# Performance work log

Hardware: AMD Instinct MI355X
Metric: run time of the kernel (lower is better)

The kernel has to match this reference:

```python
import jax, jax.numpy as jnp
import numpy as np

B, N = 32, 8192
NUM_CLASSES = 40
SA1_DIMS = (3, 64, 64, 128)      # grouped relative xyz only (in_channels=3 -> no extra features)
SA2_DIMS = (131, 128, 128, 256)  # 128 SA1 features + 3 relative xyz
LOC_DIMS = (256, 256, 512, 1024)
GLOB_DIMS = (1024, 512, 256)


def _fps(xyz, m):
    """Farthest point sampling. xyz: [B,N,3] -> indices [B,m] (first index is point 0)."""
    b, n, _ = xyz.shape
    big = jnp.asarray(1e10, xyz.dtype)

    def step(carry, _):
        dists, last = carry                                   # [B,N], [B]
        p = jnp.take_along_axis(xyz, last[:, None, None], axis=1)  # [B,1,3]
        d = jnp.sum((xyz - p) ** 2, axis=-1)                  # [B,N]
        dists = jnp.minimum(dists, d)
        nxt = jnp.argmax(dists, axis=-1).astype(jnp.int32)
        return (dists, nxt), nxt

    init = (jnp.full((b, n), big, xyz.dtype), jnp.zeros((b,), jnp.int32))
    _, rest = jax.lax.scan(step, init, None, length=m - 1)    # [m-1,B]
    return jnp.concatenate([jnp.zeros((b, 1), jnp.int32), rest.T], axis=1)


def _ball_query(xyz, new_xyz, radius, k):
    """First-k points within radius of each centroid, padded with the first hit (CUDA ball_query semantics)."""
    d2 = jnp.sum((new_xyz[:, :, None, :] - xyz[:, None, :, :]) ** 2, axis=-1)  # [B,M,N]
    valid = d2 < radius * radius
    n = xyz.shape[1]
    ar = jnp.arange(n, dtype=jnp.int32)
    order_key = jnp.where(valid, ar, ar + n)                  # valid points sort first, in index order
    _, idx = jax.lax.top_k(-order_key, k)                     # [B,M,K] first-k valid indices
    num_valid = jnp.sum(valid, axis=-1)                       # [B,M]
    idx = jnp.where(jnp.arange(k) < num_valid[..., None], idx, idx[..., :1])
    return idx.astype(jnp.int32)


_gather = jax.vmap(lambda p, i: p[i])  # p:[N,C], i:[M,K] -> [M,K,C], vmapped over batch


def _sa(xyz, feats, m, radius, k, ws, bs):
    """PointNetSAModule: FPS -> ball query -> group (relative xyz [+feat]) -> SharedMLP -> max over K."""
    cidx = _fps(xyz, m)
    new_xyz = jnp.take_along_axis(xyz, cidx[:, :, None], axis=1)   # [B,m,3]
    idx = _ball_query(xyz, new_xyz, radius, k)                     # [B,m,k]
    x = _gather(xyz, idx) - new_xyz[:, :, None, :]                 # [B,m,k,3]
    if feats is not None:
        x = jnp.concatenate([x, _gather(feats, idx)], axis=-1)
    for w, b in zip(ws, bs):  # Conv2d(1x1)+BN(eval, folded)+ReLU
        x = jax.nn.relu(jnp.einsum('bmkc,oc->bmko', x, w) + b)
    return new_xyz, jnp.max(x, axis=2)                             # [B,m,C_out]


def _forward(points, sa1_w0, sa1_b0, sa1_w1, sa1_b1, sa1_w2, sa1_b2,
             sa2_w0, sa2_b0, sa2_w1, sa2_b1, sa2_w2, sa2_b2,
             loc_w0, loc_b0, loc_w1, loc_b1, loc_w2, loc_b2,
             glob_w0, glob_b0, glob_w1, glob_b1, cls_w, cls_b):
    xyz = jnp.transpose(points, (0, 2, 1))                         # [B,N,3]
    new_xyz, feats = _sa(xyz, None, 512, 0.2, 32,
                         (sa1_w0, sa1_w1, sa1_w2), (sa1_b0, sa1_b1, sa1_b2))
    _, feats = _sa(new_xyz, feats, 128, 0.4, 64,
                   (sa2_w0, sa2_w1, sa2_w2), (sa2_b0, sa2_b1, sa2_b2))
    x = feats                                                      # [B,128,256]
    for w, b in ((loc_w0, loc_b0), (loc_w1, loc_b1), (loc_w2, loc_b2)):
        x = jax.nn.relu(jnp.einsum('bnc,oc->bno', x, w) + b)       # SharedMLP (Conv1d+BN+ReLU)
    x = jnp.max(x, axis=1)                                         # global max-pool -> [B,1024]
    for w, b in ((glob_w0, glob_b0), (glob_w1, glob_b1)):          # MLP (dropout in eval = identity)
        x = jax.nn.relu(x @ w.T + b)
    return x @ cls_w.T + cls_b                                     # cls_logits [B,40]


def setup_inputs() -> dict:
    key = jax.random.key(0)
    ks = iter(jax.random.split(key, 64))
    inp = {}
    # unit-cube point cloud so radii 0.2/0.4 are geometrically meaningful
    inp['points'] = jax.random.uniform(next(ks), (B, 3, N), jnp.float32, -1.0, 1.0)

    def lin(co, ci):
        return jax.random.normal(next(ks), (co, ci), jnp.float32) / np.sqrt(ci)

    for name, dims in (('sa1', SA1_DIMS), ('sa2', SA2_DIMS), ('loc', LOC_DIMS)):
        for i in range(len(dims) - 1):
            inp[f'{name}_w{i}'] = lin(dims[i + 1], dims[i])
            inp[f'{name}_b{i}'] = 0.01 * jax.random.normal(next(ks), (dims[i + 1],), jnp.float32)
    for i in range(2):
        inp[f'glob_w{i}'] = lin(GLOB_DIMS[i + 1], GLOB_DIMS[i])
        inp[f'glob_b{i}'] = 0.01 * jax.random.normal(next(ks), (GLOB_DIMS[i + 1],), jnp.float32)
    inp['cls_w'] = lin(NUM_CLASSES, GLOB_DIMS[-1])
    inp['cls_b'] = jnp.zeros((NUM_CLASSES,), jnp.float32)
    return inp


def reference(points, sa1_w0, sa1_b0, sa1_w1, sa1_b1, sa1_w2, sa1_b2,
              sa2_w0, sa2_b0, sa2_w1, sa2_b1, sa2_w2, sa2_b2,
              loc_w0, loc_b0, loc_w1, loc_b1, loc_w2, loc_b2,
              glob_w0, glob_b0, glob_w1, glob_b1, cls_w, cls_b):
    return _forward(points, sa1_w0, sa1_b0, sa1_w1, sa1_b1, sa1_w2, sa1_b2,
                    sa2_w0, sa2_b0, sa2_w1, sa2_b1, sa2_w2, sa2_b2,
                    loc_w0, loc_b0, loc_w1, loc_b1, loc_w2, loc_b2,
                    glob_w0, glob_b0, glob_w1, glob_b1, cls_w, cls_b)
```

## Files before the change

### kernel.cpp

```cpp
#include <hip/hip_runtime.h>
#include <hip/hip_bf16.h>
#include <cstdint>

#define CDIV(a,b) (((a)+(b)-1)/(b))

typedef short s8v __attribute__((ext_vector_type(8)));
typedef float f4v __attribute__((ext_vector_type(4)));
typedef float f2v __attribute__((ext_vector_type(2)));

__device__ __forceinline__ unsigned short f2bf_bits(float v) {
  __hip_bfloat16 b = __float2bfloat16(v);
  unsigned short u; __builtin_memcpy(&u, &b, 2);
  return u;
}
__device__ __forceinline__ void bsplit(float v, unsigned short& h, unsigned short& l) {
  __hip_bfloat16 hb = __float2bfloat16(v);
  float hf = __bfloat162float(hb);
  unsigned short hu; __builtin_memcpy(&hu, &hb, 2);
  h = hu;
  l = f2bf_bits(v - hf);
}

__device__ __forceinline__ void gl2lds16(const void* g, void* l, int lane) {
#if __has_builtin(__builtin_amdgcn_global_load_lds)
  __builtin_amdgcn_global_load_lds(
      (const __attribute__((address_space(1))) unsigned int*)g,
      (__attribute__((address_space(3))) unsigned int*)l, 16, 0, 0);
#else
  ((uint4*)l)[lane] = *(const uint4*)g;
#endif
}

__device__ __forceinline__ void agpr_put(float& slot, float v) {
  asm volatile("v_accvgpr_write_b32 %0, %1" : "=a"(slot) : "v"(v));
}
__device__ __forceinline__ float agpr_get(const float& slot) {
  float v;
  asm volatile("v_accvgpr_read_b32 %0, %1" : "=v"(v) : "a"(slot));
  return v;
}

__device__ __forceinline__ f2v pk_add(f2v a, f2v b) {
  f2v d; asm("v_pk_add_f32 %0, %1, %2" : "=v"(d) : "v"(a), "v"(b)); return d;
}
__device__ __forceinline__ f2v pk_mul(f2v a, f2v b) {
  f2v d; asm("v_pk_mul_f32 %0, %1, %2" : "=v"(d) : "v"(a), "v"(b)); return d;
}
__device__ __forceinline__ f2v pk_fma(f2v a, f2v b, f2v c) {
  f2v d; asm("v_pk_fma_f32 %0, %1, %2, %3" : "=v"(d) : "v"(a), "v"(b), "v"(c)); return d;
}

template<int C>
__device__ __forceinline__ unsigned dpp32(unsigned v) {
  return (unsigned)__builtin_amdgcn_update_dpp((int)v, (int)v, C, 0xF, 0xF, false);
}
template<int C>
__device__ __forceinline__ unsigned long long red_key(unsigned long long pk) {
  unsigned lo = dpp32<C>((unsigned)pk);
  unsigned hi = dpp32<C>((unsigned)(pk >> 32));
  unsigned long long p2 = ((unsigned long long)hi << 32) | lo;
  return (p2 > pk) ? p2 : pk;
}

template<int NPTS, int MOUT, int NTHR>
__global__ __launch_bounds__(NTHR, 1) void fps_kernel(
    const float* __restrict__ pts, int bstride, int cstride,
    int* __restrict__ out_idx)
{
  constexpr int PPT = NPTS / NTHR;
  constexpr int NP2 = PPT / 2;
  constexpr int NW  = NTHR / 64;
  const int b = blockIdx.x, t = threadIdx.x;
  const int lane = t & 63, wid = t >> 6;
  const float* px = pts + (size_t)b * bstride;
  const float* py = px + cstride;
  const float* pz = px + 2 * cstride;
  __shared__ float s_x[NPTS], s_y[NPTS], s_z[NPTS];
  __shared__ unsigned long long s_key[2][NW];
  __shared__ int s_out[MOUT];

  float ax[PPT], ay[PPT], az[PPT];
  f2v dsv[NP2];
#pragma unroll
  for (int j = 0; j < PPT; ++j) {
    int i = t + j * NTHR;
    float x = px[i], y = py[i], z = pz[i];
    s_x[i] = x; s_y[i] = y; s_z[i] = z;
    agpr_put(ax[j], x); agpr_put(ay[j], y); agpr_put(az[j], z);
  }
#pragma unroll
  for (int q = 0; q < NP2; ++q) dsv[q] = (f2v){1e10f, 1e10f};
  if (t == 0) s_out[0] = 0;
  float lx = px[0], ly = py[0], lz = pz[0];
  __syncthreads();

  for (int it = 1; it < MOUT; ++it) {
    const int pb = it & 1;
    const f2v nlx = (f2v){-lx, -lx};
    const f2v nly = (f2v){-ly, -ly};
    const f2v nlz = (f2v){-lz, -lz};
    float bestv = -1.0f; int bestj = 0;
#pragma unroll
    for (int q = 0; q < NP2; ++q) {
      f2v x2, y2, z2;
      x2.x = agpr_get(ax[2 * q]); x2.y = agpr_get(ax[2 * q + 1]);
      y2.x = agpr_get(ay[2 * q]); y2.y = agpr_get(ay[2 * q + 1]);
      z2.x = agpr_get(az[2 * q]); z2.y = agpr_get(az[2 * q + 1]);
      f2v dx = pk_add(x2, nlx);
      f2v dy = pk_add(y2, nly);
      f2v dz = pk_add(z2, nlz);
      f2v d2 = pk_fma(dz, dz, pk_fma(dy, dy, pk_mul(dx, dx)));
      float nd0 = fminf(dsv[q].x, d2.x);
      float nd1 = fminf(dsv[q].y, d2.y);
      dsv[q].x = nd0; dsv[q].y = nd1;
      if (nd0 > bestv) { bestv = nd0; bestj = 2 * q; }
      if (nd1 > bestv) { bestv = nd1; bestj = 2 * q + 1; }
    }
    const int besti = t + bestj * NTHR;
    unsigned long long pk =
        ((unsigned long long)__float_as_uint(bestv) << 32) | (unsigned)(~(unsigned)besti);
    pk = red_key<0x111>(pk);
    pk = red_key<0x112>(pk);
    pk = red_key<0x114>(pk);
    pk = red_key<0x118>(pk);
    pk = red_key<0x142>(pk);
    pk = red_key<0x143>(pk);
    if (lane == 63) s_key[pb][wid] = pk;
    __syncthreads();
    unsigned long long ck = s_key[pb][lane & (NW - 1)];
    if (NW >= 2) ck = red_key<0x111>(ck);
    if (NW >= 4) ck = red_key<0x112>(ck);
    if (NW >= 8) ck = red_key<0x114>(ck);
    const int widx = (int)(~(unsigned)__builtin_amdgcn_readlane((int)(unsigned)ck, NW - 1));
    lx = s_x[widx]; ly = s_y[widx]; lz = s_z[widx];
    if (t == 0) s_out[it] = widx;
  }
  __syncthreads();
  for (int i = t; i < MOUT; i += NTHR)
    out_idx[(size_t)b * MOUT + i] = s_out[i];
}

__global__ void gatherc_kernel(
    const float* __restrict__ pts, int bstride, int cstride,
    const int* __restrict__ cidx, int M,
    float* __restrict__ aos, float* __restrict__ soa)
{
  const int b = blockIdx.x, t = threadIdx.x;
  const int i = cidx[(size_t)b * M + t];
  const float* p = pts + (size_t)b * bstride;
  float x = p[i], y = p[cstride + i], z = p[2 * cstride + i];
  size_t g = (size_t)b * M + t;
  aos[g * 3 + 0] = x; aos[g * 3 + 1] = y; aos[g * 3 + 2] = z;
  soa[(size_t)b * 3 * M + t]         = x;
  soa[(size_t)b * 3 * M + M + t]     = y;
  soa[(size_t)b * 3 * M + 2 * M + t] = z;
}

template<int NPTS, int KNB, int MC>
__global__ __launch_bounds__(64) void ballq_wave(
    const float* __restrict__ pts, int bstride, int cstride,
    const float* __restrict__ cents, int* __restrict__ out, float r2)
{
  constexpr int NCH = NPTS / 64;
  const int g = blockIdx.x;
  const int b = g / MC;
  const int lane = threadIdx.x;
  const float* px = pts + (size_t)b * bstride;
  const float* py = px + cstride;
  const float* pz = px + 2 * cstride;
  const float cx = cents[g * 3 + 0], cy = cents[g * 3 + 1], cz = cents[g * 3 + 2];
  __shared__ int s_idx[KNB];
  float nx = px[lane], ny = py[lane], nz = pz[lane];
  int base = 0;
  for (int c = 0; c < NCH; ++c) {
    float X = nx, Y = ny, Z = nz;
    if (c + 1 < NCH) {
      int i2 = (c + 1) * 64 + lane;
      nx = px[i2]; ny = py[i2]; nz = pz[i2];
    }
    float dx = X - cx, dy = Y - cy, dz = Z - cz;
    bool valid = (dx * dx + dy * dy + dz * dz) < r2;
    unsigned long long mask = __ballot(valid);
    int rank = __popcll(mask & ((1ull << lane) - 1ull));
    int pos = base + rank;
    if (valid && pos < KNB) s_idx[pos] = c * 64 + lane;
    base += __popcll(mask);
    if (base >= KNB) break;
  }
  int total = base < KNB ? base : KNB;
  int first = s_idx[0];
  if (lane < KNB)
    out[(size_t)g * KNB + lane] = (lane < total) ? s_idx[lane] : first;
}

__global__ __launch_bounds__(256) void sa1l1_kernel(
    const float* __restrict__ pts, const int* __restrict__ idx1,
    const float* __restrict__ cents,
    const float* __restrict__ w0, const float* __restrict__ b0,
    unsigned short* __restrict__ Yh, unsigned short* __restrict__ Yl,
    int g0, int nrows)
{
  __shared__ float sw[192];
  __shared__ float sb[64];
  const int tid = threadIdx.x;
  if (tid < 192) sw[tid] = w0[tid];
  else sb[tid - 192] = b0[tid - 192];
  __syncthreads();
  const int r = blockIdx.x * 64 + (tid >> 2);
  if (r >= nrows) return;
  const int q = tid & 3;
  const int gl = r >> 5, j = r & 31, gg = g0 + gl, b = gg >> 9;
  const int i = idx1[(size_t)gg * 32 + j];
  const float* px = pts + (size_t)b * 24576;
  const float x = px[i]         - cents[gg * 3 + 0];
  const float y = px[8192 + i]  - cents[gg * 3 + 1];
  const float z = px[16384 + i] - cents[gg * 3 + 2];
  union { unsigned short us[16]; uint4 v[2]; } ph, pl;
#pragma unroll
  for (int u = 0; u < 16; ++u) {
    const int o = q * 16 + u;
    float v = sw[o * 3] * x + sw[o * 3 + 1] * y + sw[o * 3 + 2] * z + sb[o];
    v = fmaxf(v, 0.f);
    bsplit(v, ph.us[u], pl.us[u]);
  }
  uint4* dh = (uint4*)(Yh + (size_t)r * 64 + q * 16);
  uint4* dl = (uint4*)(Yl + (size_t)r * 64 + q * 16);
  dh[0] = ph.v[0]; dh[1] = ph.v[1];
  dl[0] = pl.v[0]; dl[1] = pl.v[1];
}

__global__ void gather2p_kernel(
    const float* __restrict__ nx1_aos,
    const unsigned short* __restrict__ f1h, const unsigned short* __restrict__ f1l,
    const int* __restrict__ idx2, const float* __restrict__ nx2_aos,
    unsigned short* __restrict__ Xh, unsigned short* __restrict__ Xl, int g0)
{
  const int r = blockIdx.x * 4 + threadIdx.y;
  const int lane = threadIdx.x;
  int gl = r >> 6, j = r & 63;
  int gg = g0 + gl;
  int b  = gg >> 7;
  int i  = idx2[(size_t)gg * 64 + j];
  int p  = b * 512 + i;
  size_t ro = (size_t)r * 160;
  const int slot = lane & 31;
  const bool isL = lane >= 32;
  unsigned short* dst = isL ? Xl : Xh;
  const unsigned short* f1 = isL ? f1l : f1h;
  if (slot < 16) {
    ((uint4*)(dst + ro))[slot] = ((const uint4*)(f1 + (size_t)p * 128))[slot];
  } else if (slot == 16) {
    union { unsigned short us[8]; uint4 v; } pk;
#pragma unroll
    for (int u = 0; u < 8; ++u) pk.us[u] = 0;
#pragma unroll
    for (int c = 0; c < 3; ++c) {
      float v = nx1_aos[(size_t)p * 3 + c] - nx2_aos[(size_t)gg * 3 + c];
      unsigned short h, l; bsplit(v, h, l);
      pk.us[c] = isL ? l : h;
    }
    ((uint4*)(dst + ro))[16] = pk.v;
  } else if (slot <= 19) {
    ((uint4*)(dst + ro))[slot] = make_uint4(0, 0, 0, 0);
  }
}

struct WSplitArgs {
  const float* src[9];
  unsigned short* h[9];
  unsigned short* l[9];
  int K[9];
  int KP[9];
  int perm[9];
  int cum[10];
};
__global__ void wsplit_all(WSplitArgs a) {
  int i = blockIdx.x * 256 + threadIdx.x;
  if (i >= a.cum[9]) return;
  int s = 0;
#pragma unroll
  for (int t = 1; t < 9; ++t) s += (i >= a.cum[t]);
  int local = i - a.cum[s];
  int KP = a.KP[s], K = a.K[s];
  int r = local / KP, k = local - r * KP;
  int oc;
  if (a.perm[s]) oc = (k < 128) ? k + 3 : (k < 131 ? k - 128 : -1);
  else           oc = (k < K) ? k : -1;
  float v = (oc >= 0) ? a.src[s][(size_t)r * K + oc] : 0.f;
  unsigned short hb, lb; bsplit(v, hb, lb);
  a.h[s][local] = hb; a.l[s][local] = lb;
}

template<int BN, int POOL>
__global__ __launch_bounds__(256, 1) void mfma_gemm(
    const unsigned short* __restrict__ Ah, const unsigned short* __restrict__ Al,
    const unsigned short* __restrict__ Wh, const unsigned short* __restrict__ Wl,
    const float* __restrict__ bias,
    unsigned short* __restrict__ Ch, unsigned short* __restrict__ Cl,
    float* __restrict__ Cf,
    unsigned short* __restrict__ Chp, unsigned short* __restrict__ Clp,
    int Kdim, int Ndim)
{
  constexpr int WTN = BN / 2, NT = WTN / 16;
  __shared__ unsigned short sA[2][128 * 32];
  __shared__ unsigned short sW[2][BN * 32];
  __shared__ float sPool[4][WTN];
  const int tid = threadIdx.x, lane = tid & 63, wid = tid >> 6;
  const int wm = wid & 1, wn = wid >> 1;
  const size_t bm0 = (size_t)blockIdx.y * 128;
  const int bn0 = blockIdx.x * BN;
  const int mn15 = lane & 15, kgrp = lane >> 4;

  f4v acc[4][NT];
#pragma unroll
  for (int a = 0; a < 4; ++a)
#pragma unroll
    for (int b = 0; b < NT; ++b) acc[a][b] = (f4v){0.f, 0.f, 0.f, 0.f};

  const int sc = lane & 3, srl = lane >> 2;

  for (int k0 = 0; k0 < Kdim; k0 += 32) {
#pragma unroll
    for (int hh = 0; hh < 2; ++hh) {
      const int R = wid * 32 + hh * 16;
      const int m = R + srl;
      const int kg = (sc - m - (m >> 2)) & 3;
      const size_t go = (bm0 + m) * (size_t)Kdim + k0 + kg * 8;
      gl2lds16(Ah + go, &sA[0][R * 32], lane);
      gl2lds16(Al + go, &sA[1][R * 32], lane);
    }
    if (BN == 128) {
#pragma unroll
      for (int hh = 0; hh < 2; ++hh) {
        const int R = wid * 32 + hh * 16;
        const int n = R + srl;
        const int kg = (sc - n - (n >> 2)) & 3;
        const size_t go = (size_t)(bn0 + n) * Kdim + k0 + kg * 8;
        gl2lds16(Wh + go, &sW[0][R * 32], lane);
        gl2lds16(Wl + go, &sW[1][R * 32], lane);
      }
    } else {
      const int R = wid * 16;
      const int n = R + srl;
      const int kg = (sc - n - (n >> 2)) & 3;
      const size_t go = (size_t)(bn0 + n) * Kdim + k0 + kg * 8;
      gl2lds16(Wh + go, &sW[0][R * 32], lane);
      gl2lds16(Wl + go, &sW[1][R * 32], lane);
    }
    __syncthreads();

    s8v af[2][4], bfr[2][NT];
#pragma unroll
    for (int mt = 0; mt < 4; ++mt) {
      const int m = wm * 64 + mt * 16 + mn15;
      const int cc = (kgrp + m + (m >> 2)) & 3;
      af[0][mt] = *(const s8v*)&sA[0][m * 32 + cc * 8];
      af[1][mt] = *(const s8v*)&sA[1][m * 32 + cc * 8];
    }
#pragma unroll
    for (int nt = 0; nt < NT; ++nt) {
      const int n = wn * WTN + nt * 16 + mn15;
      const int cc = (kgrp + n + (n >> 2)) & 3;
      bfr[0][nt] = *(const s8v*)&sW[0][n * 32 + cc * 8];
      bfr[1][nt] = *(const s8v*)&sW[1][n * 32 + cc * 8];
    }
#pragma unroll
    for (int mt = 0; mt < 4; ++mt)
#pragma unroll
      for (int nt = 0; nt < NT; ++nt) {
        acc[mt][nt] = __builtin_amdgcn_mfma_f32_16x16x32_bf16(af[0][mt], bfr[0][nt], acc[mt][nt], 0, 0, 0);
        acc[mt][nt] = __builtin_amdgcn_mfma_f32_16x16x32_bf16(af[0][mt], bfr[1][nt], acc[mt][nt], 0, 0, 0);
        acc[mt][nt] = __builtin_amdgcn_mfma_f32_16x16x32_bf16(af[1][mt], bfr[0][nt], acc[mt][nt], 0, 0, 0);
      }
    __syncthreads();
  }

  float bv[NT];
#pragma unroll
  for (int nt = 0; nt < NT; ++nt) bv[nt] = bias[bn0 + wn * WTN + nt * 16 + mn15];

  if (POOL == 0) {
#pragma unroll
    for (int mt = 0; mt < 4; ++mt)
#pragma unroll
      for (int nt = 0; nt < NT; ++nt) {
        const int n = bn0 + wn * WTN + nt * 16 + mn15;
#pragma unroll
        for (int r = 0; r < 4; ++r) {
          const size_t m = bm0 + wm * 64 + mt * 16 + (lane >> 4) * 4 + r;
          float v = fmaxf(acc[mt][nt][r] + bv[nt], 0.f);
          unsigned short h, l; bsplit(v, h, l);
          Ch[m * Ndim + n] = h;
          Cl[m * Ndim + n] = l;
        }
      }
  } else if (POOL == 32) {
#pragma unroll
    for (int gq = 0; gq < 2; ++gq)
#pragma unroll
      for (int nt = 0; nt < NT; ++nt) {
        float v = -1e30f;
#pragma unroll
        for (int mt = 2 * gq; mt < 2 * gq + 2; ++mt)
#pragma unroll
          for (int r = 0; r < 4; ++r) v = fmaxf(v, acc[mt][nt][r]);
        v = fmaxf(v + bv[nt], 0.f);
        v = fmaxf(v, __shfl_xor(v, 16, 64));
        v = fmaxf(v, __shfl_xor(v, 32, 64));
        if (lane < 16) {
          const int n = bn0 + wn * WTN + nt * 16 + mn15;
          const size_t row = bm0 / 32 + wm * 2 + gq;
          if (Chp) { unsigned short h, l; bsplit(v, h, l);
                     Chp[row * Ndim + n] = h; Clp[row * Ndim + n] = l; }
          if (Cf) Cf[row * Ndim + n] = v;
        }
      }
  } else if (POOL == 64) {
#pragma unroll
    for (int nt = 0; nt < NT; ++nt) {
      float v = -1e30f;
#pragma unroll
      for (int mt = 0; mt < 4; ++mt)
#pragma unroll
        for (int r = 0; r < 4; ++r) v = fmaxf(v, acc[mt][nt][r]);
      v = fmaxf(v + bv[nt], 0.f);
      v = fmaxf(v, __shfl_xor(v, 16, 64));
      v = fmaxf(v, __shfl_xor(v, 32, 64));
      if (lane < 16) {
        const int n = bn0 + wn * WTN + nt * 16 + mn15;
        const size_t row = bm0 / 64 + wm;
        if (Chp) { unsigned short h, l; bsplit(v, h, l);
                   Chp[row * Ndim + n] = h; Clp[row * Ndim + n] = l; }
        if (Cf) Cf[row * Ndim + n] = v;
      }
    }
  } else {
    float part[NT];
#pragma unroll
    for (int nt = 0; nt < NT; ++nt) {
      float v = -1e30f;
#pragma unroll
      for (int mt = 0; mt < 4; ++mt)
#pragma unroll
        for (int r = 0; r < 4; ++r) v = fmaxf(v, acc[mt][nt][r]);
      v = fmaxf(v + bv[nt], 0.f);
      v = fmaxf(v, __shfl_xor(v, 16, 64));
      v = fmaxf(v, __shfl_xor(v, 32, 64));
      part[nt] = v;
      if (lane < 16) sPool[wid][nt * 16 + mn15] = v;
    }
    __syncthreads();
    if (wm == 0 && lane < 16) {
#pragma unroll
      for (int nt = 0; nt < NT; ++nt) {
        float v = fmaxf(part[nt], sPool[wid + 1][nt * 16 + mn15]);
        const int n = bn0 + wn * WTN + nt * 16 + mn15;
        if (Cf) Cf[(size_t)(bm0 / 128) * Ndim + n] = v;
      }
    }
  }
}

__global__ __launch_bounds__(256) void head_kernel(
    const float* __restrict__ pooled,
    const float* __restrict__ w0, const float* __restrict__ b0,
    const float* __restrict__ w1, const float* __restrict__ b1,
    const float* __restrict__ wc, const float* __restrict__ bc,
    float* __restrict__ out)
{
  __shared__ float sx[1024];
  __shared__ float sy[512];
  __shared__ float sz[256];
  const int b = blockIdx.x, t = threadIdx.x;
  for (int i = t; i < 1024; i += 256) sx[i] = pooled[(size_t)b * 1024 + i];
  __syncthreads();
  for (int o = t; o < 512; o += 256) {
    const float4* w4 = (const float4*)(w0 + (size_t)o * 1024);
    const float4* x4 = (const float4*)sx;
    float acc = 0.f;
#pragma unroll 4
    for (int k = 0; k < 256; ++k) {
      float4 w = w4[k], x = x4[k];
      acc += w.x * x.x + w.y * x.y + w.z * x.z + w.w * x.w;
    }
    sy[o] = fmaxf(acc + b0[o], 0.f);
  }
  __syncthreads();
  if (t < 256) {
    const float4* w4 = (const float4*)(w1 + (size_t)t * 512);
    const float4* y4 = (const float4*)sy;
    float acc = 0.f;
#pragma unroll 4
    for (int k = 0; k < 128; ++k) {
      float4 w = w4[k], y = y4[k];
      acc += w.x * y.x + w.y * y.y + w.z * y.z + w.w * y.w;
    }
    sz[t] = fmaxf(acc + b1[t], 0.f);
  }
  __syncthreads();
  if (t < 40) {
    const float4* w4 = (const float4*)(wc + (size_t)t * 256);
    const float4* z4 = (const float4*)sz;
    float acc = 0.f;
#pragma unroll 4
    for (int k = 0; k < 64; ++k) {
      float4 w = w4[k], z = z4[k];
      acc += w.x * z.x + w.y * z.y + w.z * z.z + w.w * z.w;
    }
    out[(size_t)b * 40 + t] = acc + bc[t];
  }
}

extern "C" void kernel_launch(void* const* d_in, const int* in_sizes, int n_in,
                              void* d_out, int out_size, void* d_ws, size_t ws_size,
                              hipStream_t stream)
{
  (void)in_sizes; (void)n_in; (void)out_size; (void)ws_size;

  const float* points  = (const float*)d_in[0];
  const float* sa1_w[3] = {(const float*)d_in[1], (const float*)d_in[3], (const float*)d_in[5]};
  const float* sa1_b[3] = {(const float*)d_in[2], (const float*)d_in[4], (const float*)d_in[6]};
  const float* sa2_w[3] = {(const float*)d_in[7], (const float*)d_in[9], (const float*)d_in[11]};
  const float* sa2_b[3] = {(const float*)d_in[8], (const float*)d_in[10], (const float*)d_in[12]};
  const float* loc_w[3] = {(const float*)d_in[13], (const float*)d_in[15], (const float*)d_in[17]};
  const float* loc_b[3] = {(const float*)d_in[14], (const float*)d_in[16], (const float*)d_in[18]};
  const float* glob_w0 = (const float*)d_in[19];
  const float* glob_b0 = (const float*)d_in[20];
  const float* glob_w1 = (const float*)d_in[21];
  const float* glob_b1 = (const float*)d_in[22];
  const float* cls_w   = (const float*)d_in[23];
  const float* cls_b   = (const float*)d_in[24];

  char* base = (char*)d_ws;
  size_t off = 0;
  auto alloc = [&](size_t nbytes) -> void* {
    void* p = base + off;
    off += (nbytes + 255) & ~(size_t)255;
    return p;
  };

  const size_t XE = (size_t)65536 * 160;
  const size_t YE = (size_t)131072 * 64;
  unsigned short* Xh = (unsigned short*)alloc(XE * 2);
  unsigned short* Xl = (unsigned short*)alloc(XE * 2);
  unsigned short* Yh = (unsigned short*)alloc(YE * 2);
  unsigned short* Yl = (unsigned short*)alloc(YE * 2);
  unsigned short* f1h = (unsigned short*)alloc((size_t)16384 * 128 * 2);
  unsigned short* f1l = (unsigned short*)alloc((size_t)16384 * 128 * 2);
  unsigned short* f2h = (unsigned short*)alloc((size_t)4096 * 256 * 2);
  unsigned short* f2l = (unsigned short*)alloc((size_t)4096 * 256 * 2);

  const int  wrows[9] = {64, 64, 128, 128, 128, 256, 256, 512, 1024};
  const int  wK[9]    = {3, 64, 64, 131, 128, 128, 256, 256, 512};
  const int  wKP[9]   = {32, 64, 64, 160, 128, 128, 256, 256, 512};
  const float* wsrc[9] = {sa1_w[0], sa1_w[1], sa1_w[2],
                          sa2_w[0], sa2_w[1], sa2_w[2],
                          loc_w[0], loc_w[1], loc_w[2]};
  unsigned short *wph[9], *wpl[9];
  WSplitArgs wa;
  int cum = 0;
  for (int s = 0; s < 9; ++s) {
    size_t e = (size_t)wrows[s] * wKP[s];
    wph[s] = (unsigned short*)alloc(e * 2);
    wpl[s] = (unsigned short*)alloc(e * 2);
    wa.src[s] = wsrc[s]; wa.h[s] = wph[s]; wa.l[s] = wpl[s];
    wa.K[s] = wK[s]; wa.KP[s] = wKP[s]; wa.cum[s] = cum;
    wa.perm[s] = (s == 3) ? 1 : 0;
    cum += wrows[s] * wKP[s];
  }
  wa.cum[9] = cum;

  float* nx1_aos = (float*)alloc((size_t)32 * 512 * 3 * 4);
  float* nx1_soa = (float*)alloc((size_t)32 * 512 * 3 * 4);
  int*   cidx1   = (int*)  alloc((size_t)32 * 512 * 4);
  int*   idx1    = (int*)  alloc((size_t)32 * 512 * 32 * 4);
  float* nx2_aos = (float*)alloc((size_t)32 * 128 * 3 * 4);
  float* nx2_soa = (float*)alloc((size_t)32 * 128 * 3 * 4);
  int*   cidx2   = (int*)  alloc((size_t)32 * 128 * 4);
  int*   idx2    = (int*)  alloc((size_t)32 * 128 * 64 * 4);
  float* pooled  = (float*)alloc((size_t)32 * 1024 * 4);

  const float r2a = (float)(0.2 * 0.2);
  const float r2b = (float)(0.4 * 0.4);

  wsplit_all<<<CDIV(cum, 256), 256, 0, stream>>>(wa);

  fps_kernel<8192, 512, 512><<<32, 512, 0, stream>>>(points, 24576, 8192, cidx1);
  gatherc_kernel<<<32, 512, 0, stream>>>(points, 24576, 8192, cidx1, 512, nx1_aos, nx1_soa);
  ballq_wave<8192, 32, 512><<<32 * 512, 64, 0, stream>>>(points, 24576, 8192, nx1_aos, idx1, r2a);

  for (int c = 0; c < 4; ++c) {
    const int g0 = c * 4096;
    const int rows = 4096 * 32;
    sa1l1_kernel<<<CDIV(rows, 64), 256, 0, stream>>>(
        points, idx1, nx1_aos, sa1_w[0], sa1_b[0], Yh, Yl, g0, rows);
    mfma_gemm<64, 0><<<dim3(1, rows / 128), 256, 0, stream>>>(
        Yh, Yl, wph[1], wpl[1], sa1_b[1], Xh, Xl, nullptr, nullptr, nullptr, 64, 64);
    mfma_gemm<128, 32><<<dim3(1, rows / 128), 256, 0, stream>>>(
        Xh, Xl, wph[2], wpl[2], sa1_b[2], nullptr, nullptr, nullptr,
        f1h + (size_t)g0 * 128, f1l + (size_t)g0 * 128, 64, 128);
  }

  fps_kernel<512, 128, 256><<<32, 256, 0, stream>>>(nx1_soa, 1536, 512, cidx2);
  gatherc_kernel<<<32, 128, 0, stream>>>(nx1_soa, 1536, 512, cidx2, 128, nx2_aos, nx2_soa);
  ballq_wave<512, 64, 128><<<32 * 128, 64, 0, stream>>>(nx1_soa, 1536, 512, nx2_aos, idx2, r2b);

  for (int c = 0; c < 4; ++c) {
    const int g0 = c * 1024;
    const int rows = 1024 * 64;
    gather2p_kernel<<<dim3(rows / 4), dim3(64, 4), 0, stream>>>(
        nx1_aos, f1h, f1l, idx2, nx2_aos, Xh, Xl, g0);
    mfma_gemm<128, 0><<<dim3(1, rows / 128), 256, 0, stream>>>(
        Xh, Xl, wph[3], wpl[3], sa2_b[0], Yh, Yl, nullptr, nullptr, nullptr, 160, 128);
    mfma_gemm<128, 0><<<dim3(1, rows / 128), 256, 0, stream>>>(
        Yh, Yl, wph[4], wpl[4], sa2_b[1], Xh, Xl, nullptr, nullptr, nullptr, 128, 128);
    mfma_gemm<128, 64><<<dim3(2, rows / 128), 256, 0, stream>>>(
        Xh, Xl, wph[5], wpl[5], sa2_b[2], nullptr, nullptr, nullptr,
        f2h + (size_t)g0 * 256, f2l + (size_t)g0 * 256, 128, 256);
  }

  mfma_gemm<128, 0><<<dim3(2, 32), 256, 0, stream>>>(
      f2h, f2l, wph[6], wpl[6], loc_b[0], Yh, Yl, nullptr, nullptr, nullptr, 256, 256);
  mfma_gemm<128, 0><<<dim3(4, 32), 256, 0, stream>>>(
      Yh, Yl, wph[7], wpl[7], loc_b[1], Xh, Xl, nullptr, nullptr, nullptr, 256, 512);
  mfma_gemm<128, 128><<<dim3(8, 32), 256, 0, stream>>>(
      Xh, Xl, wph[8], wpl[8], loc_b[2], nullptr, nullptr, pooled, nullptr, nullptr, 512, 1024);

  head_kernel<<<32, 256, 0, stream>>>(pooled, glob_w0, glob_b0,
                                      glob_w1, glob_b1, cls_w, cls_b, (float*)d_out);
}
```

Measured before the change: 1.327 ms.

## Fuse SA1 MLP layers and max-pool into one kernel; single-wave FPS for SA2

Replaces the per-chunk SA1 pipeline (first-layer kernel plus two GEMM launches with global intermediates) with one kernel per 128-row tile. That kernel computes layer 0, runs both MFMA GEMMs through LDS, and max-pools over the 32 neighbours in registers. This removes global round-trips of the intermediate activations and 11 launches. It also runs the second FPS with one 64-thread wave, so the block-wide barrier and LDS reduction drop out, at the cost of less parallelism per batch.

```diff
diff --git a/kernel.cpp b/kernel.cpp
--- a/kernel.cpp
+++ b/kernel.cpp
@@ -71,7 +71,8 @@
   constexpr int NP2 = PPT / 2;
   constexpr int NW  = NTHR / 64;
   const int b = blockIdx.x, t = threadIdx.x;
-  const int lane = t & 63, wid = t >> 6;
+  const int lane = t & 63;
+  const int wid = t >> 6;
   const float* px = pts + (size_t)b * bstride;
   const float* py = px + cstride;
   const float* pz = px + 2 * cstride;
@@ -95,7 +96,6 @@
   __syncthreads();
 
   for (int it = 1; it < MOUT; ++it) {
-    const int pb = it & 1;
     const f2v nlx = (f2v){-lx, -lx};
     const f2v nly = (f2v){-ly, -ly};
     const f2v nlz = (f2v){-lz, -lz};
@@ -125,13 +125,19 @@
     pk = red_key<0x118>(pk);
     pk = red_key<0x142>(pk);
     pk = red_key<0x143>(pk);
-    if (lane == 63) s_key[pb][wid] = pk;
-    __syncthreads();
-    unsigned long long ck = s_key[pb][lane & (NW - 1)];
-    if (NW >= 2) ck = red_key<0x111>(ck);
-    if (NW >= 4) ck = red_key<0x112>(ck);
-    if (NW >= 8) ck = red_key<0x114>(ck);
-    const int widx = (int)(~(unsigned)__builtin_amdgcn_readlane((int)(unsigned)ck, NW - 1));
+    int widx;
+    if constexpr (NW == 1) {
+      widx = (int)(~(unsigned)__builtin_amdgcn_readlane((int)(unsigned)pk, 63));
+    } else {
+      const int pb = it & 1;
+      if (lane == 63) s_key[pb][wid] = pk;
+      __syncthreads();
+      unsigned long long ck = s_key[pb][lane & (NW - 1)];
+      if (NW >= 2) ck = red_key<0x111>(ck);
+      if (NW >= 4) ck = red_key<0x112>(ck);
+      if (NW >= 8) ck = red_key<0x114>(ck);
+      widx = (int)(~(unsigned)__builtin_amdgcn_readlane((int)(unsigned)ck, NW - 1));
+    }
     lx = s_x[widx]; ly = s_y[widx]; lz = s_z[widx];
     if (t == 0) s_out[it] = widx;
   }
@@ -193,40 +199,172 @@
     out[(size_t)g * KNB + lane] = (lane < total) ? s_idx[lane] : first;
 }
 
-__global__ __launch_bounds__(256) void sa1l1_kernel(
+__global__ __launch_bounds__(256, 1) void sa1_fused(
     const float* __restrict__ pts, const int* __restrict__ idx1,
     const float* __restrict__ cents,
     const float* __restrict__ w0, const float* __restrict__ b0,
-    unsigned short* __restrict__ Yh, unsigned short* __restrict__ Yl,
-    int g0, int nrows)
+    const unsigned short* __restrict__ w1h, const unsigned short* __restrict__ w1l,
+    const float* __restrict__ b1,
+    const unsigned short* __restrict__ w2h, const unsigned short* __restrict__ w2l,
+    const float* __restrict__ b2,
+    unsigned short* __restrict__ f1h, unsigned short* __restrict__ f1l)
 {
-  __shared__ float sw[192];
-  __shared__ float sb[64];
-  const int tid = threadIdx.x;
-  if (tid < 192) sw[tid] = w0[tid];
-  else sb[tid - 192] = b0[tid - 192];
-  __syncthreads();
-  const int r = blockIdx.x * 64 + (tid >> 2);
-  if (r >= nrows) return;
-  const int q = tid & 3;
-  const int gl = r >> 5, j = r & 31, gg = g0 + gl, b = gg >> 9;
-  const int i = idx1[(size_t)gg * 32 + j];
-  const float* px = pts + (size_t)b * 24576;
-  const float x = px[i]         - cents[gg * 3 + 0];
-  const float y = px[8192 + i]  - cents[gg * 3 + 1];
-  const float z = px[16384 + i] - cents[gg * 3 + 2];
-  union { unsigned short us[16]; uint4 v[2]; } ph, pl;
-#pragma unroll
-  for (int u = 0; u < 16; ++u) {
-    const int o = q * 16 + u;
-    float v = sw[o * 3] * x + sw[o * 3 + 1] * y + sw[o * 3 + 2] * z + sb[o];
-    v = fmaxf(v, 0.f);
-    bsplit(v, ph.us[u], pl.us[u]);
-  }
-  uint4* dh = (uint4*)(Yh + (size_t)r * 64 + q * 16);
-  uint4* dl = (uint4*)(Yl + (size_t)r * 64 + q * 16);
-  dh[0] = ph.v[0]; dh[1] = ph.v[1];
-  dl[0] = pl.v[0]; dl[1] = pl.v[1];
+  __shared__ __align__(16) unsigned short sY[2][128 * 72];
+  __shared__ __align__(16) unsigned short sZ[2][128 * 72];
+  __shared__ __align__(16) unsigned short sW[2][64 * 72];
+  __shared__ float sw0[192];
+  __shared__ float sb0[64];
+
+  const int tid = threadIdx.x, lane = tid & 63, wid = tid >> 6;
+  const int wm = wid & 1, wn = wid >> 1;
+  const int mn15 = lane & 15, kgrp = lane >> 4;
+  const int bk = blockIdx.x;
+
+  if (tid < 192) sw0[tid] = w0[tid];
+  else sb0[tid - 192] = b0[tid - 192];
+  for (int gi = tid; gi < 1024; gi += 256) {
+    const int pl = gi >> 9, idx = gi & 511;
+    const int n = idx >> 3, k8 = idx & 7;
+    const uint4 v = ((const uint4*)(pl ? w1l : w1h))[idx];
+    *(uint4*)&sW[pl][n * 72 + k8 * 8] = v;
+  }
+  __syncthreads();
+
+  {
+    const int rl = tid >> 1, half = tid & 1;
+    const int r = bk * 128 + rl;
+    const int gl = r >> 5, j = r & 31, b = gl >> 9;
+    const int i = idx1[(size_t)gl * 32 + j];
+    const float* px = pts + (size_t)b * 24576;
+    const float x = px[i]         - cents[gl * 3 + 0];
+    const float y = px[8192 + i]  - cents[gl * 3 + 1];
+    const float z = px[16384 + i] - cents[gl * 3 + 2];
+    union { unsigned short us[32]; uint4 v[4]; } ph, pl4;
+#pragma unroll
+    for (int u = 0; u < 32; ++u) {
+      const int o = half * 32 + u;
+      float v = sw0[o * 3] * x + sw0[o * 3 + 1] * y + sw0[o * 3 + 2] * z + sb0[o];
+      v = fmaxf(v, 0.f);
+      bsplit(v, ph.us[u], pl4.us[u]);
+    }
+    const int base = rl * 72 + half * 32;
+#pragma unroll
+    for (int g = 0; g < 4; ++g) {
+      *(uint4*)&sY[0][base + g * 8] = ph.v[g];
+      *(uint4*)&sY[1][base + g * 8] = pl4.v[g];
+    }
+  }
+  __syncthreads();
+
+  {
+    f4v acc[4][2];
+#pragma unroll
+    for (int a = 0; a < 4; ++a)
+#pragma unroll
+      for (int c = 0; c < 2; ++c) acc[a][c] = (f4v){0.f, 0.f, 0.f, 0.f};
+#pragma unroll
+    for (int kc = 0; kc < 2; ++kc) {
+      const int k0 = kc * 32;
+      s8v af[2][4], bf[2][2];
+#pragma unroll
+      for (int mt = 0; mt < 4; ++mt) {
+        const int m = wm * 64 + mt * 16 + mn15;
+        af[0][mt] = *(const s8v*)&sY[0][m * 72 + k0 + kgrp * 8];
+        af[1][mt] = *(const s8v*)&sY[1][m * 72 + k0 + kgrp * 8];
+      }
+#pragma unroll
+      for (int nt = 0; nt < 2; ++nt) {
+        const int n = wn * 32 + nt * 16 + mn15;
+        bf[0][nt] = *(const s8v*)&sW[0][n * 72 + k0 + kgrp * 8];
+        bf[1][nt] = *(const s8v*)&sW[1][n * 72 + k0 + kgrp * 8];
+      }
+#pragma unroll
+      for (int mt = 0; mt < 4; ++mt)
+#pragma unroll
+        for (int nt = 0; nt < 2; ++nt) {
+          acc[mt][nt] = __builtin_amdgcn_mfma_f32_16x16x32_bf16(af[0][mt], bf[0][nt], acc[mt][nt], 0, 0, 0);
+          acc[mt][nt] = __builtin_amdgcn_mfma_f32_16x16x32_bf16(af[0][mt], bf[1][nt], acc[mt][nt], 0, 0, 0);
+          acc[mt][nt] = __builtin_amdgcn_mfma_f32_16x16x32_bf16(af[1][mt], bf[0][nt], acc[mt][nt], 0, 0, 0);
+        }
+    }
+#pragma unroll
+    for (int nt = 0; nt < 2; ++nt) {
+      const int n = wn * 32 + nt * 16 + mn15;
+      const float bv = b1[n];
+#pragma unroll
+      for (int mt = 0; mt < 4; ++mt)
+#pragma unroll
+        for (int r = 0; r < 4; ++r) {
+          const int m = wm * 64 + mt * 16 + (lane >> 4) * 4 + r;
+          float v = fmaxf(acc[mt][nt][r] + bv, 0.f);
+          unsigned short h, l; bsplit(v, h, l);
+          sZ[0][m * 72 + n] = h;
+          sZ[1][m * 72 + n] = l;
+        }
+    }
+  }
+  __syncthreads();
+
+  for (int gi = tid; gi < 2048; gi += 256) {
+    const int pl = gi >> 10, idx = gi & 1023;
+    const int n = idx >> 3, k8 = idx & 7;
+    const uint4 v = ((const uint4*)(pl ? w2l : w2h))[idx];
+    *(uint4*)&sY[pl][n * 72 + k8 * 8] = v;
+  }
+  __syncthreads();
+
+  {
+    f4v acc[4][4];
+#pragma unroll
+    for (int a = 0; a < 4; ++a)
+#pragma unroll
+      for (int c = 0; c < 4; ++c) acc[a][c] = (f4v){0.f, 0.f, 0.f, 0.f};
+#pragma unroll
+    for (int kc = 0; kc < 2; ++kc) {
+      const int k0 = kc * 32;
+      s8v af[2][4], bf[2][4];
+#pragma unroll
+      for (int mt = 0; mt < 4; ++mt) {
+        const int m = wm * 64 + mt * 16 + mn15;
+        af[0][mt] = *(const s8v*)&sZ[0][m * 72 + k0 + kgrp * 8];
+        af[1][mt] = *(const s8v*)&sZ[1][m * 72 + k0 + kgrp * 8];
+      }
+#pragma unroll
+      for (int nt = 0; nt < 4; ++nt) {
+        const int n = wn * 64 + nt * 16 + mn15;
+        bf[0][nt] = *(const s8v*)&sY[0][n * 72 + k0 + kgrp * 8];
+        bf[1][nt] = *(const s8v*)&sY[1][n * 72 + k0 + kgrp * 8];
+      }
+#pragma unroll
+      for (int mt = 0; mt < 4; ++mt)
+#pragma unroll
+        for (int nt = 0; nt < 4; ++nt) {
+          acc[mt][nt] = __builtin_amdgcn_mfma_f32_16x16x32_bf16(af[0][mt], bf[0][nt], acc[mt][nt], 0, 0, 0);
+          acc[mt][nt] = __builtin_amdgcn_mfma_f32_16x16x32_bf16(af[0][mt], bf[1][nt], acc[mt][nt], 0, 0, 0);
+          acc[mt][nt] = __builtin_amdgcn_mfma_f32_16x16x32_bf16(af[1][mt], bf[0][nt], acc[mt][nt], 0, 0, 0);
+        }
+    }
+#pragma unroll
+    for (int gq = 0; gq < 2; ++gq)
+#pragma unroll
+      for (int nt = 0; nt < 4; ++nt) {
+        const int n = wn * 64 + nt * 16 + mn15;
+        float v = -1e30f;
+#pragma unroll
+        for (int mt = 2 * gq; mt < 2 * gq + 2; ++mt)
+#pragma unroll
+          for (int r = 0; r < 4; ++r) v = fmaxf(v, acc[mt][nt][r]);
+        v = fmaxf(v + b2[n], 0.f);
+        v = fmaxf(v, __shfl_xor(v, 16, 64));
+        v = fmaxf(v, __shfl_xor(v, 32, 64));
+        if (lane < 16) {
+          const size_t row = (size_t)bk * 4 + wm * 2 + gq;
+          unsigned short h, l; bsplit(v, h, l);
+          f1h[row * 128 + n] = h;
+          f1l[row * 128 + n] = l;
+        }
+      }
+  }
 }
 
 __global__ void gather2p_kernel(
@@ -589,19 +727,11 @@
   gatherc_kernel<<<32, 512, 0, stream>>>(points, 24576, 8192, cidx1, 512, nx1_aos, nx1_soa);
   ballq_wave<8192, 32, 512><<<32 * 512, 64, 0, stream>>>(points, 24576, 8192, nx1_aos, idx1, r2a);
 
-  for (int c = 0; c < 4; ++c) {
-    const int g0 = c * 4096;
-    const int rows = 4096 * 32;
-    sa1l1_kernel<<<CDIV(rows, 64), 256, 0, stream>>>(
-        points, idx1, nx1_aos, sa1_w[0], sa1_b[0], Yh, Yl, g0, rows);
-    mfma_gemm<64, 0><<<dim3(1, rows / 128), 256, 0, stream>>>(
-        Yh, Yl, wph[1], wpl[1], sa1_b[1], Xh, Xl, nullptr, nullptr, nullptr, 64, 64);
-    mfma_gemm<128, 32><<<dim3(1, rows / 128), 256, 0, stream>>>(
-        Xh, Xl, wph[2], wpl[2], sa1_b[2], nullptr, nullptr, nullptr,
-        f1h + (size_t)g0 * 128, f1l + (size_t)g0 * 128, 64, 128);
-  }
-
-  fps_kernel<512, 128, 256><<<32, 256, 0, stream>>>(nx1_soa, 1536, 512, cidx2);
+  sa1_fused<<<4096, 256, 0, stream>>>(
+      points, idx1, nx1_aos, sa1_w[0], sa1_b[0],
+      wph[1], wpl[1], sa1_b[1], wph[2], wpl[2], sa1_b[2], f1h, f1l);
+
+  fps_kernel<512, 128, 64><<<32, 64, 0, stream>>>(nx1_soa, 1536, 512, cidx2);
   gatherc_kernel<<<32, 128, 0, stream>>>(nx1_soa, 1536, 512, cidx2, 128, nx2_aos, nx2_soa);
   ballq_wave<512, 64, 128><<<32 * 128, 64, 0, stream>>>(nx1_soa, 1536, 512, nx2_aos, idx2, r2b);
 
```

After: 1.286 ms. 3.1% less time.
